# Kernel tuning notes

Hardware: AMD Instinct MI355X
Metric: run time of the kernel (lower is better)

## Reference

```python
import jax, jax.numpy as jnp
import numpy as np

IN_FEATURES = 128
OUT_FEATURES = 32
N_NODES = 2048
ALPHA = 0.2  # LeakyReLU negative slope
NEG_INF = -9e15


def setup_inputs() -> dict:
    key = jax.random.key(0)
    k1, k2, k3, k4 = jax.random.split(key, 4)
    h = jax.random.normal(k1, (N_NODES, IN_FEATURES), dtype=jnp.float32)
    adj = jax.random.randint(k2, (N_NODES, N_NODES), 0, 2, dtype=jnp.int32)
    # xavier_uniform-ish scaling for params
    W = jax.random.normal(k3, (2 * IN_FEATURES, OUT_FEATURES), dtype=jnp.float32) * 0.1
    a = jax.random.normal(k4, (OUT_FEATURES,), dtype=jnp.float32) * 0.2
    return {"h": h, "adj": adj, "W": W, "a": a}


def reference(h, adj, W, a):
    in_f = h.shape[1]
    Wh1 = h @ W[:in_f, :]   # [N, F]
    Wh2 = h @ W[in_f:, :]   # [N, F]
    # GATv2 score: e[i,k] = sum_f a[f] * leaky_relu(Wh1[i,f] + Wh2[k,f])
    e = jax.nn.leaky_relu(Wh1[:, None, :] + Wh2[None, :, :], negative_slope=ALPHA)  # [N, N, F]
    e = jnp.einsum('ikf,f->ik', e, a)  # [N, N]
    att = jnp.where(adj > 0, e, NEG_INF)
    att = jax.nn.softmax(att, axis=1)
    h_prime = att @ Wh1  # note: original aggregates Wh1, faithful to source
    return jax.nn.elu(h_prime)  # concat=True -> ELU
```

## Files before the change

kernel.cpp:

```cpp
#include <hip/hip_runtime.h>
#include <math.h>

#define N_NODES 2048
#define IN_F 128
#define OUT_F 32
#define NEG_INF -9e15f

__device__ __forceinline__ int swz(int k) { return k ^ (((k >> 7) & 7) << 2); }

__global__ __launch_bounds__(256) void precompute_wh(
    const float* __restrict__ h, const float* __restrict__ W,
    const float* __restrict__ a,
    float* __restrict__ Wh1, float* __restrict__ Wh2T,
    float* __restrict__ Q, float* __restrict__ C)
{
    __shared__ float h_s[8][IN_F];
    __shared__ float tr[8][OUT_F];
    const int t = threadIdx.x;
    const int i0 = blockIdx.x * 8;

    ((float4*)&h_s[0][0])[t] = ((const float4*)(h + (size_t)i0 * IN_F))[t];
    __syncthreads();

    const int f = t & 31;
    const int r = t >> 5;
    float acc1 = 0.f, acc2 = 0.f;
    #pragma unroll 8
    for (int c = 0; c < IN_F; ++c) {
        const float hv = h_s[r][c];
        acc1 = fmaf(hv, W[c * OUT_F + f], acc1);
        acc2 = fmaf(hv, W[(IN_F + c) * OUT_F + f], acc2);
    }
    Wh1[(i0 + r) * OUT_F + f] = acc1;
    tr[r][f] = acc2;

    float q = 0.6f * a[f] * acc2;
    #pragma unroll
    for (int off = 16; off > 0; off >>= 1) q += __shfl_xor(q, off, 64);
    if (f == 0) Q[i0 + r] = q;
    if (blockIdx.x == 0 && t < OUT_F) C[t] = 0.4f * a[t];

    __syncthreads();
    const int f2 = t >> 3, r2 = t & 7;
    Wh2T[f2 * N_NODES + i0 + r2] = tr[r2][f2];
}

__global__ __launch_bounds__(256, 2) void gat_row(
    const float* __restrict__ Wh1, const float* __restrict__ Wh2T,
    const float* __restrict__ Q, const float* __restrict__ C,
    const int* __restrict__ adj, float* __restrict__ out)
{
    __shared__ float p_s[4][N_NODES];
    __shared__ float w1s[4][OUT_F];
    __shared__ float part[16][4][OUT_F];
    __shared__ float redM[4][4], redL[4][4];

    const int t = threadIdx.x;
    const int i0 = blockIdx.x * 4;

    if (t < 4 * OUT_F) w1s[t >> 5][t & 31] = Wh1[i0 * OUT_F + t];
    __syncthreads();

    const int kA = 4 * t;
    const int kB = N_NODES / 2 + 4 * t;

    int4 adA[4], adB[4];
    #pragma unroll
    for (int i = 0; i < 4; ++i) {
        adA[i] = *(const int4*)(adj + (size_t)(i0 + i) * N_NODES + kA);
        adB[i] = *(const int4*)(adj + (size_t)(i0 + i) * N_NODES + kB);
    }
    const float4 QA = *(const float4*)(Q + kA);
    const float4 QB = *(const float4*)(Q + kB);

    float acc[4][8];
    #pragma unroll
    for (int i = 0; i < 4; ++i)
        #pragma unroll
        for (int s = 0; s < 8; ++s) acc[i][s] = 0.f;

    #pragma unroll 2
    for (int j = 0; j < 8; ++j) {
        float4 w1v[4];
        #pragma unroll
        for (int i = 0; i < 4; ++i) w1v[i] = *(const float4*)&w1s[i][4 * j];
        #pragma unroll
        for (int e = 0; e < 4; ++e) {
            const int f = 4 * j + e;
            const float cf = C[f];
            const float4 wA = *(const float4*)(Wh2T + (size_t)f * N_NODES + kA);
            const float4 wB = *(const float4*)(Wh2T + (size_t)f * N_NODES + kB);
            #pragma unroll
            for (int i = 0; i < 4; ++i) {
                const float w1 = (e==0)?w1v[i].x:(e==1)?w1v[i].y:(e==2)?w1v[i].z:w1v[i].w;
                acc[i][0] = fmaf(cf, fabsf(w1 + wA.x), acc[i][0]);
                acc[i][1] = fmaf(cf, fabsf(w1 + wA.y), acc[i][1]);
                acc[i][2] = fmaf(cf, fabsf(w1 + wA.z), acc[i][2]);
                acc[i][3] = fmaf(cf, fabsf(w1 + wA.w), acc[i][3]);
                acc[i][4] = fmaf(cf, fabsf(w1 + wB.x), acc[i][4]);
                acc[i][5] = fmaf(cf, fabsf(w1 + wB.y), acc[i][5]);
                acc[i][6] = fmaf(cf, fabsf(w1 + wB.z), acc[i][6]);
                acc[i][7] = fmaf(cf, fabsf(w1 + wB.w), acc[i][7]);
            }
        }
    }

    float m[4];
    #pragma unroll
    for (int i = 0; i < 4; ++i) {
        acc[i][0] = (adA[i].x > 0) ? acc[i][0] + QA.x : NEG_INF;
        acc[i][1] = (adA[i].y > 0) ? acc[i][1] + QA.y : NEG_INF;
        acc[i][2] = (adA[i].z > 0) ? acc[i][2] + QA.z : NEG_INF;
        acc[i][3] = (adA[i].w > 0) ? acc[i][3] + QA.w : NEG_INF;
        acc[i][4] = (adB[i].x > 0) ? acc[i][4] + QB.x : NEG_INF;
        acc[i][5] = (adB[i].y > 0) ? acc[i][5] + QB.y : NEG_INF;
        acc[i][6] = (adB[i].z > 0) ? acc[i][6] + QB.z : NEG_INF;
        acc[i][7] = (adB[i].w > 0) ? acc[i][7] + QB.w : NEG_INF;
        float mm = fmaxf(fmaxf(fmaxf(acc[i][0], acc[i][1]), fmaxf(acc[i][2], acc[i][3])),
                         fmaxf(fmaxf(acc[i][4], acc[i][5]), fmaxf(acc[i][6], acc[i][7])));
        #pragma unroll
        for (int off = 32; off > 0; off >>= 1) mm = fmaxf(mm, __shfl_xor(mm, off, 64));
        m[i] = mm;
    }
    const int lane = t & 63, wid = t >> 6;
    if (lane == 0) {
        redM[0][wid] = m[0]; redM[1][wid] = m[1];
        redM[2][wid] = m[2]; redM[3][wid] = m[3];
    }
    __syncthreads();

    float L[4];
    #pragma unroll
    for (int i = 0; i < 4; ++i) {
        const float M = fmaxf(fmaxf(redM[i][0], redM[i][1]), fmaxf(redM[i][2], redM[i][3]));
        const float p0 = __expf(acc[i][0] - M);
        const float p1 = __expf(acc[i][1] - M);
        const float p2 = __expf(acc[i][2] - M);
        const float p3 = __expf(acc[i][3] - M);
        const float p4 = __expf(acc[i][4] - M);
        const float p5 = __expf(acc[i][5] - M);
        const float p6 = __expf(acc[i][6] - M);
        const float p7 = __expf(acc[i][7] - M);
        *(float4*)&p_s[i][swz(kA)] = make_float4(p0, p1, p2, p3);
        *(float4*)&p_s[i][swz(kB)] = make_float4(p4, p5, p6, p7);
        float ll = (p0 + p1) + (p2 + p3) + ((p4 + p5) + (p6 + p7));
        #pragma unroll
        for (int off = 32; off > 0; off >>= 1) ll += __shfl_xor(ll, off, 64);
        L[i] = ll;
    }
    if (lane == 0) {
        redL[0][wid] = L[0]; redL[1][wid] = L[1];
        redL[2][wid] = L[2]; redL[3][wid] = L[3];
    }
    __syncthreads();

    const int f2 = t & 15;
    const int c  = t >> 4;
    float a00=0.f, a01=0.f, a10=0.f, a11=0.f, a20=0.f, a21=0.f, a30=0.f, a31=0.f;
    const int kb = c * 128;
    #pragma unroll 4
    for (int it = 0; it < 32; ++it) {
        const int k = kb + 4 * it;
        const int ks = swz(k);
        const float4 p0 = *(const float4*)&p_s[0][ks];
        const float4 p1 = *(const float4*)&p_s[1][ks];
        const float4 p2 = *(const float4*)&p_s[2][ks];
        const float4 p3 = *(const float4*)&p_s[3][ks];
        const float* wrow = Wh1 + (size_t)k * OUT_F + f2;
        const float wa0 = wrow[0],  wb0 = wrow[16];
        const float wa1 = wrow[32], wb1 = wrow[48];
        const float wa2 = wrow[64], wb2 = wrow[80];
        const float wa3 = wrow[96], wb3 = wrow[112];
        a00 = fmaf(p0.x, wa0, a00); a01 = fmaf(p0.x, wb0, a01);
        a10 = fmaf(p1.x, wa0, a10); a11 = fmaf(p1.x, wb0, a11);
        a20 = fmaf(p2.x, wa0, a20); a21 = fmaf(p2.x, wb0, a21);
        a30 = fmaf(p3.x, wa0, a30); a31 = fmaf(p3.x, wb0, a31);
        a00 = fmaf(p0.y, wa1, a00); a01 = fmaf(p0.y, wb1, a01);
        a10 = fmaf(p1.y, wa1, a10); a11 = fmaf(p1.y, wb1, a11);
        a20 = fmaf(p2.y, wa1, a20); a21 = fmaf(p2.y, wb1, a21);
        a30 = fmaf(p3.y, wa1, a30); a31 = fmaf(p3.y, wb1, a31);
        a00 = fmaf(p0.z, wa2, a00); a01 = fmaf(p0.z, wb2, a01);
        a10 = fmaf(p1.z, wa2, a10); a11 = fmaf(p1.z, wb2, a11);
        a20 = fmaf(p2.z, wa2, a20); a21 = fmaf(p2.z, wb2, a21);
        a30 = fmaf(p3.z, wa2, a30); a31 = fmaf(p3.z, wb2, a31);
        a00 = fmaf(p0.w, wa3, a00); a01 = fmaf(p0.w, wb3, a01);
        a10 = fmaf(p1.w, wa3, a10); a11 = fmaf(p1.w, wb3, a11);
        a20 = fmaf(p2.w, wa3, a20); a21 = fmaf(p2.w, wb3, a21);
        a30 = fmaf(p3.w, wa3, a30); a31 = fmaf(p3.w, wb3, a31);
    }
    part[c][0][f2] = a00; part[c][0][f2 + 16] = a01;
    part[c][1][f2] = a10; part[c][1][f2 + 16] = a11;
    part[c][2][f2] = a20; part[c][2][f2 + 16] = a21;
    part[c][3][f2] = a30; part[c][3][f2 + 16] = a31;
    __syncthreads();

    if (t < 4 * OUT_F) {
        const int ii = t >> 5, ff = t & 31;
        float s = 0.f;
        #pragma unroll
        for (int c2 = 0; c2 < 16; ++c2) s += part[c2][ii][ff];
        const float Lf = redL[ii][0] + redL[ii][1] + redL[ii][2] + redL[ii][3];
        const float val = s / Lf;
        out[(i0 + ii) * OUT_F + ff] = (val > 0.f) ? val : (__expf(val) - 1.f);
    }
}

extern "C" void kernel_launch(void* const* d_in, const int* in_sizes, int n_in,
                              void* d_out, int out_size, void* d_ws, size_t ws_size,
                              hipStream_t stream) {
    const float* h   = (const float*)d_in[0];
    const int*   adj = (const int*)d_in[1];
    const float* W   = (const float*)d_in[2];
    const float* a   = (const float*)d_in[3];
    float* out = (float*)d_out;

    float* Wh1  = (float*)d_ws;
    float* Wh2T = Wh1 + N_NODES * OUT_F;
    float* Q    = Wh2T + N_NODES * OUT_F;
    float* C    = Q + N_NODES;

    precompute_wh<<<N_NODES / 8, 256, 0, stream>>>(h, W, a, Wh1, Wh2T, Q, C);
    gat_row<<<N_NODES / 4, 256, 0, stream>>>(Wh1, Wh2T, Q, C, adj, out);
}
```

Baseline: 102.5 us.

## Process eight rows per 1024-thread block with two-phase shared-memory aggregation

```diff
diff --git a/kernel.cpp b/kernel.cpp
--- a/kernel.cpp
+++ b/kernel.cpp
@@ -5,8 +5,13 @@
 #define IN_F 128
 #define OUT_F 32
 #define NEG_INF -9e15f
-
-__device__ __forceinline__ int swz(int k) { return k ^ (((k >> 7) & 7) << 2); }
+#define TI 8
+#define NT 1024
+
+__device__ __forceinline__ int pw(int k, int ih) {
+    const int S = ((k >> 1) ^ (k >> 4)) & 7;
+    return ((k << 3) | (ih << 2)) ^ (S << 2);
+}
 
 __global__ __launch_bounds__(256) void precompute_wh(
     const float* __restrict__ h, const float* __restrict__ W,
@@ -45,163 +50,152 @@
     Wh2T[f2 * N_NODES + i0 + r2] = tr[r2][f2];
 }
 
-__global__ __launch_bounds__(256, 2) void gat_row(
+__global__ __launch_bounds__(NT) void gat_row(
     const float* __restrict__ Wh1, const float* __restrict__ Wh2T,
     const float* __restrict__ Q, const float* __restrict__ C,
     const int* __restrict__ adj, float* __restrict__ out)
 {
-    __shared__ float p_s[4][N_NODES];
-    __shared__ float w1s[4][OUT_F];
-    __shared__ float part[16][4][OUT_F];
-    __shared__ float redM[4][4], redL[4][4];
+    __shared__ __align__(16) float p_s[8 * (N_NODES / 2)];
+    __shared__ __align__(16) float w1s[TI][OUT_F];
+    __shared__ __align__(16) float part[16][TI][OUT_F];
+    __shared__ float redM[TI][16], redL[TI][16], Mfin[TI];
 
     const int t = threadIdx.x;
-    const int i0 = blockIdx.x * 4;
-
-    if (t < 4 * OUT_F) w1s[t >> 5][t & 31] = Wh1[i0 * OUT_F + t];
-    __syncthreads();
-
-    const int kA = 4 * t;
-    const int kB = N_NODES / 2 + 4 * t;
-
-    int4 adA[4], adB[4];
-    #pragma unroll
-    for (int i = 0; i < 4; ++i) {
-        adA[i] = *(const int4*)(adj + (size_t)(i0 + i) * N_NODES + kA);
-        adB[i] = *(const int4*)(adj + (size_t)(i0 + i) * N_NODES + kB);
-    }
-    const float4 QA = *(const float4*)(Q + kA);
-    const float4 QB = *(const float4*)(Q + kB);
-
-    float acc[4][8];
-    #pragma unroll
-    for (int i = 0; i < 4; ++i)
-        #pragma unroll
-        for (int s = 0; s < 8; ++s) acc[i][s] = 0.f;
-
-    #pragma unroll 2
+    const int i0 = blockIdx.x * TI;
+    const int k0 = 2 * t;
+    const int lane = t & 63, wid = t >> 6;
+
+    if (t < TI * OUT_F) w1s[t >> 5][t & 31] = Wh1[i0 * OUT_F + t];
+    __syncthreads();
+
+    int2 ad[TI];
+    #pragma unroll
+    for (int i = 0; i < TI; ++i)
+        ad[i] = *(const int2*)(adj + (size_t)(i0 + i) * N_NODES + k0);
+    const float2 q2 = *(const float2*)(Q + k0);
+
+    float acc0[TI], acc1[TI];
+    #pragma unroll
+    for (int i = 0; i < TI; ++i) { acc0[i] = 0.f; acc1[i] = 0.f; }
+
+    #pragma unroll 4
     for (int j = 0; j < 8; ++j) {
-        float4 w1v[4];
-        #pragma unroll
-        for (int i = 0; i < 4; ++i) w1v[i] = *(const float4*)&w1s[i][4 * j];
-        #pragma unroll
-        for (int e = 0; e < 4; ++e) {
-            const int f = 4 * j + e;
-            const float cf = C[f];
-            const float4 wA = *(const float4*)(Wh2T + (size_t)f * N_NODES + kA);
-            const float4 wB = *(const float4*)(Wh2T + (size_t)f * N_NODES + kB);
-            #pragma unroll
-            for (int i = 0; i < 4; ++i) {
-                const float w1 = (e==0)?w1v[i].x:(e==1)?w1v[i].y:(e==2)?w1v[i].z:w1v[i].w;
-                acc[i][0] = fmaf(cf, fabsf(w1 + wA.x), acc[i][0]);
-                acc[i][1] = fmaf(cf, fabsf(w1 + wA.y), acc[i][1]);
-                acc[i][2] = fmaf(cf, fabsf(w1 + wA.z), acc[i][2]);
-                acc[i][3] = fmaf(cf, fabsf(w1 + wA.w), acc[i][3]);
-                acc[i][4] = fmaf(cf, fabsf(w1 + wB.x), acc[i][4]);
-                acc[i][5] = fmaf(cf, fabsf(w1 + wB.y), acc[i][5]);
-                acc[i][6] = fmaf(cf, fabsf(w1 + wB.z), acc[i][6]);
-                acc[i][7] = fmaf(cf, fabsf(w1 + wB.w), acc[i][7]);
-            }
-        }
-    }
-
-    float m[4];
-    #pragma unroll
-    for (int i = 0; i < 4; ++i) {
-        acc[i][0] = (adA[i].x > 0) ? acc[i][0] + QA.x : NEG_INF;
-        acc[i][1] = (adA[i].y > 0) ? acc[i][1] + QA.y : NEG_INF;
-        acc[i][2] = (adA[i].z > 0) ? acc[i][2] + QA.z : NEG_INF;
-        acc[i][3] = (adA[i].w > 0) ? acc[i][3] + QA.w : NEG_INF;
-        acc[i][4] = (adB[i].x > 0) ? acc[i][4] + QB.x : NEG_INF;
-        acc[i][5] = (adB[i].y > 0) ? acc[i][5] + QB.y : NEG_INF;
-        acc[i][6] = (adB[i].z > 0) ? acc[i][6] + QB.z : NEG_INF;
-        acc[i][7] = (adB[i].w > 0) ? acc[i][7] + QB.w : NEG_INF;
-        float mm = fmaxf(fmaxf(fmaxf(acc[i][0], acc[i][1]), fmaxf(acc[i][2], acc[i][3])),
-                         fmaxf(fmaxf(acc[i][4], acc[i][5]), fmaxf(acc[i][6], acc[i][7])));
-        #pragma unroll
-        for (int off = 32; off > 0; off >>= 1) mm = fmaxf(mm, __shfl_xor(mm, off, 64));
-        m[i] = mm;
-    }
-    const int lane = t & 63, wid = t >> 6;
-    if (lane == 0) {
-        redM[0][wid] = m[0]; redM[1][wid] = m[1];
-        redM[2][wid] = m[2]; redM[3][wid] = m[3];
-    }
-    __syncthreads();
-
-    float L[4];
-    #pragma unroll
-    for (int i = 0; i < 4; ++i) {
-        const float M = fmaxf(fmaxf(redM[i][0], redM[i][1]), fmaxf(redM[i][2], redM[i][3]));
-        const float p0 = __expf(acc[i][0] - M);
-        const float p1 = __expf(acc[i][1] - M);
-        const float p2 = __expf(acc[i][2] - M);
-        const float p3 = __expf(acc[i][3] - M);
-        const float p4 = __expf(acc[i][4] - M);
-        const float p5 = __expf(acc[i][5] - M);
-        const float p6 = __expf(acc[i][6] - M);
-        const float p7 = __expf(acc[i][7] - M);
-        *(float4*)&p_s[i][swz(kA)] = make_float4(p0, p1, p2, p3);
-        *(float4*)&p_s[i][swz(kB)] = make_float4(p4, p5, p6, p7);
-        float ll = (p0 + p1) + (p2 + p3) + ((p4 + p5) + (p6 + p7));
-        #pragma unroll
-        for (int off = 32; off > 0; off >>= 1) ll += __shfl_xor(ll, off, 64);
-        L[i] = ll;
-    }
-    if (lane == 0) {
-        redL[0][wid] = L[0]; redL[1][wid] = L[1];
-        redL[2][wid] = L[2]; redL[3][wid] = L[3];
-    }
-    __syncthreads();
-
-    const int f2 = t & 15;
-    const int c  = t >> 4;
-    float a00=0.f, a01=0.f, a10=0.f, a11=0.f, a20=0.f, a21=0.f, a30=0.f, a31=0.f;
-    const int kb = c * 128;
-    #pragma unroll 4
-    for (int it = 0; it < 32; ++it) {
-        const int k = kb + 4 * it;
-        const int ks = swz(k);
-        const float4 p0 = *(const float4*)&p_s[0][ks];
-        const float4 p1 = *(const float4*)&p_s[1][ks];
-        const float4 p2 = *(const float4*)&p_s[2][ks];
-        const float4 p3 = *(const float4*)&p_s[3][ks];
-        const float* wrow = Wh1 + (size_t)k * OUT_F + f2;
-        const float wa0 = wrow[0],  wb0 = wrow[16];
-        const float wa1 = wrow[32], wb1 = wrow[48];
-        const float wa2 = wrow[64], wb2 = wrow[80];
-        const float wa3 = wrow[96], wb3 = wrow[112];
-        a00 = fmaf(p0.x, wa0, a00); a01 = fmaf(p0.x, wb0, a01);
-        a10 = fmaf(p1.x, wa0, a10); a11 = fmaf(p1.x, wb0, a11);
-        a20 = fmaf(p2.x, wa0, a20); a21 = fmaf(p2.x, wb0, a21);
-        a30 = fmaf(p3.x, wa0, a30); a31 = fmaf(p3.x, wb0, a31);
-        a00 = fmaf(p0.y, wa1, a00); a01 = fmaf(p0.y, wb1, a01);
-        a10 = fmaf(p1.y, wa1, a10); a11 = fmaf(p1.y, wb1, a11);
-        a20 = fmaf(p2.y, wa1, a20); a21 = fmaf(p2.y, wb1, a21);
-        a30 = fmaf(p3.y, wa1, a30); a31 = fmaf(p3.y, wb1, a31);
-        a00 = fmaf(p0.z, wa2, a00); a01 = fmaf(p0.z, wb2, a01);
-        a10 = fmaf(p1.z, wa2, a10); a11 = fmaf(p1.z, wb2, a11);
-        a20 = fmaf(p2.z, wa2, a20); a21 = fmaf(p2.z, wb2, a21);
-        a30 = fmaf(p3.z, wa2, a30); a31 = fmaf(p3.z, wb2, a31);
-        a00 = fmaf(p0.w, wa3, a00); a01 = fmaf(p0.w, wb3, a01);
-        a10 = fmaf(p1.w, wa3, a10); a11 = fmaf(p1.w, wb3, a11);
-        a20 = fmaf(p2.w, wa3, a20); a21 = fmaf(p2.w, wb3, a21);
-        a30 = fmaf(p3.w, wa3, a30); a31 = fmaf(p3.w, wb3, a31);
-    }
-    part[c][0][f2] = a00; part[c][0][f2 + 16] = a01;
-    part[c][1][f2] = a10; part[c][1][f2 + 16] = a11;
-    part[c][2][f2] = a20; part[c][2][f2 + 16] = a21;
-    part[c][3][f2] = a30; part[c][3][f2 + 16] = a31;
-    __syncthreads();
-
-    if (t < 4 * OUT_F) {
-        const int ii = t >> 5, ff = t & 31;
+        float2 w2[4];
+        #pragma unroll
+        for (int e = 0; e < 4; ++e)
+            w2[e] = *(const float2*)(Wh2T + (size_t)(4 * j + e) * N_NODES + k0);
+        const float c0 = C[4 * j + 0], c1 = C[4 * j + 1];
+        const float c2 = C[4 * j + 2], c3 = C[4 * j + 3];
+        #pragma unroll
+        for (int i = 0; i < TI; ++i) {
+            const float4 w1 = *(const float4*)&w1s[i][4 * j];
+            float x;
+            x = w1.x + w2[0].x; acc0[i] = fmaf(c0, fabsf(x), acc0[i]);
+            x = w1.x + w2[0].y; acc1[i] = fmaf(c0, fabsf(x), acc1[i]);
+            x = w1.y + w2[1].x; acc0[i] = fmaf(c1, fabsf(x), acc0[i]);
+            x = w1.y + w2[1].y; acc1[i] = fmaf(c1, fabsf(x), acc1[i]);
+            x = w1.z + w2[2].x; acc0[i] = fmaf(c2, fabsf(x), acc0[i]);
+            x = w1.z + w2[2].y; acc1[i] = fmaf(c2, fabsf(x), acc1[i]);
+            x = w1.w + w2[3].x; acc0[i] = fmaf(c3, fabsf(x), acc0[i]);
+            x = w1.w + w2[3].y; acc1[i] = fmaf(c3, fabsf(x), acc1[i]);
+        }
+    }
+
+    #pragma unroll
+    for (int i = 0; i < TI; ++i) {
+        acc0[i] = (ad[i].x > 0) ? acc0[i] + q2.x : NEG_INF;
+        acc1[i] = (ad[i].y > 0) ? acc1[i] + q2.y : NEG_INF;
+        float mm = fmaxf(acc0[i], acc1[i]);
+        #pragma unroll
+        for (int off = 32; off > 0; off >>= 1)
+            mm = fmaxf(mm, __shfl_xor(mm, off, 64));
+        if (lane == 0) redM[i][wid] = mm;
+    }
+    __syncthreads();
+    if (t < 128) {
+        float v = redM[t >> 4][t & 15];
+        #pragma unroll
+        for (int off = 8; off > 0; off >>= 1)
+            v = fmaxf(v, __shfl_xor(v, off, 64));
+        if ((t & 15) == 0) Mfin[t >> 4] = v;
+    }
+    __syncthreads();
+
+    float pr0[TI], pr1[TI];
+    #pragma unroll
+    for (int i = 0; i < TI; ++i) {
+        const float M = Mfin[i];
+        pr0[i] = __expf(acc0[i] - M);
+        pr1[i] = __expf(acc1[i] - M);
+        float ll = pr0[i] + pr1[i];
+        #pragma unroll
+        for (int off = 32; off > 0; off >>= 1)
+            ll += __shfl_xor(ll, off, 64);
+        if (lane == 0) redL[i][wid] = ll;
+    }
+
+    const int fq = (t & 7) * 4;
+    const int c  = t >> 3;
+    float4 av[TI];
+    #pragma unroll
+    for (int i = 0; i < TI; ++i) av[i] = make_float4(0.f, 0.f, 0.f, 0.f);
+
+    #pragma unroll
+    for (int h = 0; h < 2; ++h) {
+        __syncthreads();
+        if ((t >> 9) == h) {
+            const int kl = 2 * (t & 511);
+            *(float4*)&p_s[pw(kl, 0)]     = make_float4(pr0[0], pr0[1], pr0[2], pr0[3]);
+            *(float4*)&p_s[pw(kl, 1)]     = make_float4(pr0[4], pr0[5], pr0[6], pr0[7]);
+            *(float4*)&p_s[pw(kl + 1, 0)] = make_float4(pr1[0], pr1[1], pr1[2], pr1[3]);
+            *(float4*)&p_s[pw(kl + 1, 1)] = make_float4(pr1[4], pr1[5], pr1[6], pr1[7]);
+        }
+        __syncthreads();
+        #pragma unroll
+        for (int it = 0; it < 8; ++it) {
+            const int kl = 8 * c + it;
+            const int kg = h * (N_NODES / 2) + kl;
+            const float4 w  = *(const float4*)(Wh1 + (size_t)kg * OUT_F + fq);
+            const float4 pA = *(const float4*)&p_s[pw(kl, 0)];
+            const float4 pB = *(const float4*)&p_s[pw(kl, 1)];
+            #define ACC(ii, pv) \
+                av[ii].x = fmaf(pv, w.x, av[ii].x); \
+                av[ii].y = fmaf(pv, w.y, av[ii].y); \
+                av[ii].z = fmaf(pv, w.z, av[ii].z); \
+                av[ii].w = fmaf(pv, w.w, av[ii].w);
+            ACC(0, pA.x) ACC(1, pA.y) ACC(2, pA.z) ACC(3, pA.w)
+            ACC(4, pB.x) ACC(5, pB.y) ACC(6, pB.z) ACC(7, pB.w)
+            #undef ACC
+        }
+    }
+
+    #pragma unroll
+    for (int off = 8; off <= 32; off <<= 1) {
+        #pragma unroll
+        for (int i = 0; i < TI; ++i) {
+            av[i].x += __shfl_xor(av[i].x, off, 64);
+            av[i].y += __shfl_xor(av[i].y, off, 64);
+            av[i].z += __shfl_xor(av[i].z, off, 64);
+            av[i].w += __shfl_xor(av[i].w, off, 64);
+        }
+    }
+    if (lane < 8) {
+        #pragma unroll
+        for (int i = 0; i < TI; ++i)
+            *(float4*)&part[wid][i][fq] = av[i];
+    }
+    __syncthreads();
+
+    if (t < TI * OUT_F) {
+        const int i = t >> 5, f = t & 31;
         float s = 0.f;
         #pragma unroll
-        for (int c2 = 0; c2 < 16; ++c2) s += part[c2][ii][ff];
-        const float Lf = redL[ii][0] + redL[ii][1] + redL[ii][2] + redL[ii][3];
-        const float val = s / Lf;
-        out[(i0 + ii) * OUT_F + ff] = (val > 0.f) ? val : (__expf(val) - 1.f);
+        for (int w = 0; w < 16; ++w) s += part[w][i][f];
+        float L = 0.f;
+        #pragma unroll
+        for (int w = 0; w < 16; ++w) L += redL[i][w];
+        const float val = s / L;
+        out[(i0 + i) * OUT_F + f] = (val > 0.f) ? val : (__expf(val) - 1.f);
     }
 }
 
@@ -220,5 +214,5 @@
     float* C    = Q + N_NODES;
 
     precompute_wh<<<N_NODES / 8, 256, 0, stream>>>(h, W, a, Wh1, Wh2T, Q, C);
-    gat_row<<<N_NODES / 4, 256, 0, stream>>>(Wh1, Wh2T, Q, C, adj, out);
-}
+    gat_row<<<N_NODES / TI, NT, 0, stream>>>(Wh1, Wh2T, Q, C, adj, out);
+}
```

Measured after the change: 101.1 us. About the same (-1.4%).
